# Kernel tuning notes

Measured on AMD Instinct MI355X. Metric: run time of the kernel, lower is better.

Reference implementation:

```python
import jax, jax.numpy as jnp
import numpy as np

N = 50000        # nodes
E = 1_600_000    # edges (avg degree 32)
F_IN = 128       # node feature dim
H = 64           # hidden_channels
C = 19           # output classes
G = 512          # graphs in the batch


def setup_inputs() -> dict:
    key = jax.random.key(0)
    ks = jax.random.split(key, 9)
    x = jax.random.normal(ks[0], (N, F_IN), dtype=jnp.float32)
    edge_index = jax.random.randint(ks[1], (2, E), 0, N, dtype=jnp.int64)
    batch = jnp.sort(jax.random.randint(ks[2], (N,), 0, G, dtype=jnp.int64))
    W1 = jax.random.normal(ks[3], (F_IN, H), dtype=jnp.float32) / np.sqrt(F_IN)
    b1 = jnp.zeros((H,), dtype=jnp.float32)
    W2 = jax.random.normal(ks[4], (H, H), dtype=jnp.float32) / np.sqrt(H)
    b2 = jnp.zeros((H,), dtype=jnp.float32)
    W_out = jax.random.normal(ks[5], (H, C), dtype=jnp.float32) / np.sqrt(H)
    b_out = jnp.zeros((C,), dtype=jnp.float32)
    return {"x": x, "edge_index": edge_index, "batch": batch,
            "W1": W1, "b1": b1, "W2": W2, "b2": b2,
            "W_out": W_out, "b_out": b_out}


def _gcn_conv(x, src, dst, W, b, n_nodes):
    """PyG GCNConv: add self-loops, symmetric D^-1/2 (A+I) D^-1/2 norm,
    linear transform first, gather-scale-scatter aggregation, then bias."""
    x = x @ W  # [N, out]
    loop = jnp.arange(n_nodes, dtype=src.dtype)
    s = jnp.concatenate([src, loop])  # source (message origin)
    d = jnp.concatenate([dst, loop])  # target (aggregation site)
    deg = jax.ops.segment_sum(jnp.ones_like(d, dtype=x.dtype), d,
                              num_segments=n_nodes)
    dinv = jnp.where(deg > 0, jax.lax.rsqrt(deg), 0.0)
    norm = dinv[s] * dinv[d]                       # [E+N]
    msg = x[s] * norm[:, None]                     # gather + scale
    out = jax.ops.segment_sum(msg, d, num_segments=n_nodes)  # scatter-add
    return out + b


def reference(x, edge_index, batch, W1, b1, W2, b2, W_out, b_out):
    src, dst = edge_index[0], edge_index[1]
    h = _gcn_conv(x, src, dst, W1, b1, N)
    h = jax.nn.relu(h)
    # F.dropout(training=False) -> identity (eval mode)
    h = _gcn_conv(h, src, dst, W2, b2, N)
    # global mean pool over graphs
    sums = jax.ops.segment_sum(h, batch, num_segments=G)        # [G, H]
    cnts = jax.ops.segment_sum(jnp.ones((N,), h.dtype), batch,
                               num_segments=G)                  # [G]
    pooled = sums / jnp.maximum(cnts, 1.0)[:, None]
    return pooled @ W_out + b_out                               # [G, C]
```

## Files before the change

kernel.cpp:

```cpp
#include <hip/hip_runtime.h>
#include <hip/hip_bf16.h>

#define F_IN 128
#define HID  64
#define NCLS 19
#define BW   128
#define NBMAX 512
#define ACAP 3072
#define BCAP 8192
#define BKCAP 5120
#define W1STR 136
#define W2STR 72

typedef __bf16 bf16x8 __attribute__((ext_vector_type(8)));
typedef float  f32x4  __attribute__((ext_vector_type(4)));

__device__ __forceinline__ float ldf(const void* p, long i, int fp32) {
    if (fp32) return ((const float*)p)[i];
    return __bfloat162float(((const __hip_bfloat16*)p)[i]);
}
__device__ __forceinline__ int ldi(const void* p, long i, int i64) {
    if (i64) return (int)((const long long*)p)[i];
    return ((const int*)p)[i];
}
__device__ __forceinline__ unsigned short f2bf(float f) {
    __hip_bfloat16 h = __float2bfloat16(f);
    unsigned short r;
    __builtin_memcpy(&r, &h, 2);
    return r;
}
__device__ __forceinline__ float bflo(unsigned u) { return __uint_as_float(u << 16); }
__device__ __forceinline__ float bfhi(unsigned u) { return __uint_as_float(u & 0xffff0000u); }

__device__ __forceinline__ bf16x8 ldfrag(const unsigned short* p) {
    uint4 u = *(const uint4*)p;
    return __builtin_bit_cast(bf16x8, u);
}
__device__ __forceinline__ bf16x8 ldfrag_any(const void* p, long off, int fp32) {
    if (!fp32) return ldfrag((const unsigned short*)p + off);
    const float* f = (const float*)p + off;
    unsigned short s[8];
#pragma unroll
    for (int i = 0; i < 8; ++i) s[i] = f2bf(f[i]);
    uint4 u = make_uint4((unsigned)s[0] | ((unsigned)s[1] << 16),
                         (unsigned)s[2] | ((unsigned)s[3] << 16),
                         (unsigned)s[4] | ((unsigned)s[5] << 16),
                         (unsigned)s[6] | ((unsigned)s[7] << 16));
    return __builtin_bit_cast(bf16x8, u);
}

__global__ __launch_bounds__(512) void k_detect(const void* x, const void* ei, int* flags,
                                                int* __restrict__ bcur, int NB) {
    int t = threadIdx.x;
    for (int b = t; b < NB; b += 512) bcur[b] = b * BKCAP;
    if (t != 0) return;
    const unsigned* xw = (const unsigned*)x;
    int bf16 = 1;
    for (int i = 0; i < 16; ++i) {
        unsigned w = xw[i];
        int elo = (w >> 7) & 0xFF;
        int ehi = (w >> 23) & 0xFF;
        if (elo < 100 || elo > 140 || ehi < 100 || ehi > 140) bf16 = 0;
    }
    const unsigned* iw = (const unsigned*)ei;
    int i64 = 1; unsigned anyev = 0;
    for (int k = 0; k < 8; ++k) {
        if (iw[2 * k + 1] != 0) i64 = 0;
        anyev |= iw[2 * k];
    }
    if (anyev == 0) i64 = 0;
    flags[0] = bf16 ? 0 : 1;
    flags[1] = i64;
}

__global__ __launch_bounds__(256) void k_bounds(const void* __restrict__ batch, int N, int G,
                                                int* __restrict__ bounds,
                                                const int* __restrict__ flags) {
    int i64 = flags[1];
    int i = blockIdx.x * 256 + threadIdx.x;
    if (i >= N) return;
    int b = min(max(ldi(batch, i, i64), 0), G - 1);
    int p = (i == 0) ? -1 : min(max(ldi(batch, (long)i - 1, i64), 0), G - 1);
    for (int g = p + 1; g <= b; ++g) bounds[g] = i;
    if (i == N - 1)
        for (int g = b + 1; g <= G; ++g) bounds[g] = N;
}

__global__ __launch_bounds__(512) void k_sortA(const void* __restrict__ ei, int E, int nbuck,
                                               int* bcur, int* __restrict__ bkt,
                                               const int* __restrict__ flags) {
    __shared__ int lbuf[ACAP];
    __shared__ unsigned short lbkt[ACAP];
    __shared__ int lh[NBMAX];
    __shared__ int lsc[NBMAX];
    __shared__ int lcur[NBMAX];
    __shared__ int gbase[NBMAX];
    int i64 = flags[1];
    int t = threadIdx.x;
    int e0 = blockIdx.x * ACAP;
    int e1 = min(E, e0 + ACAP);
    int cnt = e1 - e0;
    lh[t] = 0;
    __syncthreads();
    for (int e = e0 + t; e < e1; e += 512)
        atomicAdd(&lh[(ldi(ei, (long)E + e, i64) >> 7) & (NBMAX - 1)], 1);
    __syncthreads();
    int v = lh[t];
    lsc[t] = v;
    __syncthreads();
    for (int off = 1; off < 512; off <<= 1) {
        int a = (t >= off) ? lsc[t - off] : 0;
        __syncthreads();
        lsc[t] += a;
        __syncthreads();
    }
    int ex = lsc[t] - v;
    lsc[t] = ex;
    lcur[t] = ex;
    gbase[t] = (v && t < nbuck) ? atomicAdd(&bcur[t], v) : 0;
    __syncthreads();
    for (int e = e0 + t; e < e1; e += 512) {
        int s = ldi(ei, e, i64);
        int d = ldi(ei, (long)E + e, i64);
        int b = (d >> 7) & (NBMAX - 1);
        int r = atomicAdd(&lcur[b], 1);
        r = min(max(r, 0), ACAP - 1);
        lbuf[r] = (s << 7) | (d & (BW - 1));
        lbkt[r] = (unsigned short)b;
    }
    __syncthreads();
    for (int i = t; i < cnt; i += 512) {
        int lo = lbkt[i];
        int idx = gbase[lo] + (i - lsc[lo]);
        if (idx >= lo * BKCAP && idx < (lo + 1) * BKCAP) bkt[idx] = lbuf[i];
    }
}

__global__ __launch_bounds__(256) void k_sortB(const int* __restrict__ bkt,
                                               const int* __restrict__ bcur,
                                               int N,
                                               int* __restrict__ csr,
                                               int* __restrict__ cursor,
                                               int* __restrict__ deg,
                                               float* __restrict__ dinv) {
    __shared__ int lcsr[BCAP];
    __shared__ int lh[BW], lsc[BW], lcur[BW];
    int b = blockIdx.x, t = threadIdx.x;
    int base = b * BKCAP;
    int cnt = min(max(bcur[b] - base, 0), BKCAP);
    int end = base + cnt;
    if (t < BW) lh[t] = 0;
    __syncthreads();
    for (int i = base + t; i < end; i += 256)
        atomicAdd(&lh[bkt[i] & (BW - 1)], 1);
    __syncthreads();
    if (t < BW) lsc[t] = lh[t];
    __syncthreads();
    for (int off = 1; off < BW; off <<= 1) {
        int a = (t < BW && t >= off) ? lsc[t - off] : 0;
        __syncthreads();
        if (t < BW) lsc[t] += a;
        __syncthreads();
    }
    if (t < BW) {
        int ex = lsc[t] - lh[t];
        lcur[t] = ex;
        int n = b * BW + t;
        if (n < N) {
            cursor[n] = base + ex;
            deg[n] = lh[t];
            dinv[n] = rsqrtf((float)(lh[t] + 1));
        }
    }
    __syncthreads();
    bool fits = (cnt <= BCAP);
    for (int i = base + t; i < end; i += 256) {
        int w = bkt[i];
        int r = atomicAdd(&lcur[w & (BW - 1)], 1);
        int sv = (int)((unsigned)w >> 7);
        if (sv >= N) sv = 0;
        if (fits) { r = min(max(r, 0), BCAP - 1); lcsr[r] = sv; }
        else { r = min(max(r, 0), BKCAP - 1); csr[base + r] = sv; }
    }
    __syncthreads();
    if (fits)
        for (int i = t; i < cnt; i += 256) csr[base + i] = lcsr[i];
}

__global__ __launch_bounds__(256) void k_gemm1(const void* __restrict__ x,
                                               const void* __restrict__ W,
                                               const float* __restrict__ dinv,
                                               unsigned short* __restrict__ t, int N,
                                               const int* __restrict__ flags) {
    __shared__ __align__(16) unsigned short wt[HID * W1STR];
    int fp32 = flags[0];
    int tid = threadIdx.x;
    for (int i = tid; i < F_IN * HID; i += 256) {
        int k = i >> 6, n = i & 63;
        wt[n * W1STR + k] = f2bf(ldf(W, i, fp32));
    }
    __syncthreads();
    int wv = tid >> 6, lane = tid & 63;
    int quad = lane >> 4, l16 = lane & 15;
    int r0 = blockIdx.x * 64 + wv * 16;
    int rowA = min(r0 + l16, N - 1);
    bf16x8 a[4];
#pragma unroll
    for (int kq = 0; kq < 4; ++kq)
        a[kq] = ldfrag_any(x, (long)rowA * F_IN + kq * 32 + quad * 8, fp32);
    float di[4];
    int rowC = r0 + quad * 4;
#pragma unroll
    for (int r = 0; r < 4; ++r) di[r] = (rowC + r < N) ? dinv[rowC + r] : 0.f;
#pragma unroll
    for (int cg = 0; cg < 4; ++cg) {
        int col = cg * 16 + l16;
        f32x4 acc = {0.f, 0.f, 0.f, 0.f};
#pragma unroll
        for (int kq = 0; kq < 4; ++kq) {
            bf16x8 b = ldfrag(wt + col * W1STR + kq * 32 + quad * 8);
            acc = __builtin_amdgcn_mfma_f32_16x16x32_bf16(a[kq], b, acc, 0, 0, 0);
        }
#pragma unroll
        for (int r = 0; r < 4; ++r) {
            int row = rowC + r;
            if (row < N) t[(size_t)row * HID + col] = f2bf(di[r] * acc[r]);
        }
    }
}

__global__ __launch_bounds__(256) void k_gemm2(const unsigned short* __restrict__ h,
                                               const void* __restrict__ W,
                                               const float* __restrict__ dinv,
                                               unsigned short* __restrict__ t, int N,
                                               const int* __restrict__ flags) {
    __shared__ __align__(16) unsigned short wt[HID * W2STR];
    int fp32 = flags[0];
    int tid = threadIdx.x;
    for (int i = tid; i < HID * HID; i += 256) {
        int k = i >> 6, n = i & 63;
        wt[n * W2STR + k] = f2bf(ldf(W, i, fp32));
    }
    __syncthreads();
    int wv = tid >> 6, lane = tid & 63;
    int quad = lane >> 4, l16 = lane & 15;
    int r0 = blockIdx.x * 64 + wv * 16;
    int rowA = min(r0 + l16, N - 1);
    bf16x8 a[2];
#pragma unroll
    for (int kq = 0; kq < 2; ++kq)
        a[kq] = ldfrag(h + (size_t)rowA * HID + kq * 32 + quad * 8);
    float di[4];
    int rowC = r0 + quad * 4;
#pragma unroll
    for (int r = 0; r < 4; ++r) di[r] = (rowC + r < N) ? dinv[rowC + r] : 0.f;
#pragma unroll
    for (int cg = 0; cg < 4; ++cg) {
        int col = cg * 16 + l16;
        f32x4 acc = {0.f, 0.f, 0.f, 0.f};
#pragma unroll
        for (int kq = 0; kq < 2; ++kq) {
            bf16x8 b = ldfrag(wt + col * W2STR + kq * 32 + quad * 8);
            acc = __builtin_amdgcn_mfma_f32_16x16x32_bf16(a[kq], b, acc, 0, 0, 0);
        }
#pragma unroll
        for (int r = 0; r < 4; ++r) {
            int row = rowC + r;
            if (row < N) t[(size_t)row * HID + col] = f2bf(di[r] * acc[r]);
        }
    }
}

template <bool RELU>
__global__ __launch_bounds__(256) void k_agg(const unsigned short* __restrict__ t,
                                             const int* __restrict__ csr,
                                             const int* __restrict__ cursor,
                                             const int* __restrict__ deg,
                                             const float* __restrict__ dinv,
                                             const void* __restrict__ bias,
                                             unsigned short* __restrict__ out,
                                             int N, int SZ, const int* __restrict__ flags) {
    int node = blockIdx.x * 4 + (threadIdx.x >> 6);
    if (node >= N) return;
    int lane = threadIdx.x & 63;
    int g = lane >> 3;
    int l8 = (lane & 7) * 8;
    int beg = cursor[node];
    int dg = deg[node];
    beg = min(max(beg, 0), SZ);
    int end = beg + min(max(dg, 0), SZ - beg);
    float a0 = 0.f, a1 = 0.f, a2 = 0.f, a3 = 0.f;
    float a4 = 0.f, a5 = 0.f, a6 = 0.f, a7 = 0.f;
    for (int e = beg; e < end; e += 32) {
        int i0 = e + g, i1 = e + 8 + g, i2 = e + 16 + g, i3 = e + 24 + g;
        int s0 = csr[i0 < end ? i0 : end - 1];
        int s1 = csr[i1 < end ? i1 : end - 1];
        int s2 = csr[i2 < end ? i2 : end - 1];
        int s3 = csr[i3 < end ? i3 : end - 1];
        s0 = ((unsigned)s0 < (unsigned)N) ? s0 : 0;
        s1 = ((unsigned)s1 < (unsigned)N) ? s1 : 0;
        s2 = ((unsigned)s2 < (unsigned)N) ? s2 : 0;
        s3 = ((unsigned)s3 < (unsigned)N) ? s3 : 0;
        uint4 v0 = *(const uint4*)(t + s0 * HID + l8);
        uint4 v1 = *(const uint4*)(t + s1 * HID + l8);
        uint4 v2 = *(const uint4*)(t + s2 * HID + l8);
        uint4 v3 = *(const uint4*)(t + s3 * HID + l8);
        if (i0 < end) {
            a0 += bflo(v0.x); a1 += bfhi(v0.x); a2 += bflo(v0.y); a3 += bfhi(v0.y);
            a4 += bflo(v0.z); a5 += bfhi(v0.z); a6 += bflo(v0.w); a7 += bfhi(v0.w);
        }
        if (i1 < end) {
            a0 += bflo(v1.x); a1 += bfhi(v1.x); a2 += bflo(v1.y); a3 += bfhi(v1.y);
            a4 += bflo(v1.z); a5 += bfhi(v1.z); a6 += bflo(v1.w); a7 += bfhi(v1.w);
        }
        if (i2 < end) {
            a0 += bflo(v2.x); a1 += bfhi(v2.x); a2 += bflo(v2.y); a3 += bfhi(v2.y);
            a4 += bflo(v2.z); a5 += bfhi(v2.z); a6 += bflo(v2.w); a7 += bfhi(v2.w);
        }
        if (i3 < end) {
            a0 += bflo(v3.x); a1 += bfhi(v3.x); a2 += bflo(v3.y); a3 += bfhi(v3.y);
            a4 += bflo(v3.z); a5 += bfhi(v3.z); a6 += bflo(v3.w); a7 += bfhi(v3.w);
        }
    }
#pragma unroll
    for (int m = 8; m <= 32; m <<= 1) {
        a0 += __shfl_xor(a0, m); a1 += __shfl_xor(a1, m);
        a2 += __shfl_xor(a2, m); a3 += __shfl_xor(a3, m);
        a4 += __shfl_xor(a4, m); a5 += __shfl_xor(a5, m);
        a6 += __shfl_xor(a6, m); a7 += __shfl_xor(a7, m);
    }
    uint4 sv = *(const uint4*)(t + node * HID + l8);
    a0 += bflo(sv.x); a1 += bfhi(sv.x); a2 += bflo(sv.y); a3 += bfhi(sv.y);
    a4 += bflo(sv.z); a5 += bfhi(sv.z); a6 += bflo(sv.w); a7 += bfhi(sv.w);
    int fp32 = flags[0];
    float di = dinv[node];
    float v0 = di * a0 + ldf(bias, l8 + 0, fp32);
    float v1 = di * a1 + ldf(bias, l8 + 1, fp32);
    float v2 = di * a2 + ldf(bias, l8 + 2, fp32);
    float v3 = di * a3 + ldf(bias, l8 + 3, fp32);
    float v4 = di * a4 + ldf(bias, l8 + 4, fp32);
    float v5 = di * a5 + ldf(bias, l8 + 5, fp32);
    float v6 = di * a6 + ldf(bias, l8 + 6, fp32);
    float v7 = di * a7 + ldf(bias, l8 + 7, fp32);
    if (RELU) {
        v0 = fmaxf(v0, 0.f); v1 = fmaxf(v1, 0.f); v2 = fmaxf(v2, 0.f); v3 = fmaxf(v3, 0.f);
        v4 = fmaxf(v4, 0.f); v5 = fmaxf(v5, 0.f); v6 = fmaxf(v6, 0.f); v7 = fmaxf(v7, 0.f);
    }
    if (g == 0) {
        uint4 pk;
        pk.x = (unsigned)f2bf(v0) | ((unsigned)f2bf(v1) << 16);
        pk.y = (unsigned)f2bf(v2) | ((unsigned)f2bf(v3) << 16);
        pk.z = (unsigned)f2bf(v4) | ((unsigned)f2bf(v5) << 16);
        pk.w = (unsigned)f2bf(v6) | ((unsigned)f2bf(v7) << 16);
        *(uint4*)(out + node * HID + l8) = pk;
    }
}

__global__ __launch_bounds__(64) void k_poolout(const unsigned short* __restrict__ h2,
                                                const int* __restrict__ bounds, int N,
                                                const void* __restrict__ Wout,
                                                const void* __restrict__ bout,
                                                void* __restrict__ out,
                                                const int* __restrict__ flags) {
    __shared__ float pr[HID];
    int g = blockIdx.x;
    int start = min(max(bounds[g], 0), N);
    int endg = min(max(bounds[g + 1], start), N);
    int lane = threadIdx.x;
    int half = lane >> 5;
    int l = lane & 31;
    float s0 = 0.f, s1 = 0.f;
    for (int r = start; r < endg; r += 4) {
        int r0 = r + half;
        int r1 = r + 2 + half;
        unsigned u0 = (r0 < endg) ? *(const unsigned*)(h2 + (size_t)r0 * HID + 2 * l) : 0u;
        unsigned u1 = (r1 < endg) ? *(const unsigned*)(h2 + (size_t)r1 * HID + 2 * l) : 0u;
        s0 += bflo(u0) + bflo(u1);
        s1 += bfhi(u0) + bfhi(u1);
    }
    s0 += __shfl_xor(s0, 32);
    s1 += __shfl_xor(s1, 32);
    if (lane < 32) {
        float inv = 1.f / fmaxf((float)(endg - start), 1.f);
        pr[2 * l] = s0 * inv;
        pr[2 * l + 1] = s1 * inv;
    }
    __syncthreads();
    int fp32 = flags[0];
    if (lane < NCLS) {
        float acc = ldf(bout, lane, fp32);
#pragma unroll 4
        for (int k = 0; k < HID; ++k)
            acc += pr[k] * ldf(Wout, k * NCLS + lane, fp32);
        if (fp32) ((float*)out)[g * NCLS + lane] = acc;
        else ((__hip_bfloat16*)out)[g * NCLS + lane] = __float2bfloat16(acc);
    }
}

extern "C" void kernel_launch(void* const* d_in, const int* in_sizes, int n_in,
                              void* d_out, int out_size, void* d_ws, size_t ws_size,
                              hipStream_t stream) {
    const void* x    = d_in[0];
    const void* ei   = d_in[1];
    const void* bat  = d_in[2];
    const void* W1   = d_in[3];
    const void* b1   = d_in[4];
    const void* W2   = d_in[5];
    const void* b2   = d_in[6];
    const void* Wout = d_in[7];
    const void* bout = d_in[8];

    const int N = in_sizes[0] / F_IN;
    const int E = in_sizes[1] / 2;
    const int G = out_size / NCLS;
    const int NB = (N + BW - 1) / BW;
    const int SZ = NB * BKCAP;

    char* ws = (char*)d_ws;
    size_t off = 0;
    auto carve = [&](size_t bytes) -> void* {
        void* p = ws + off;
        off = (off + bytes + 255) & ~(size_t)255;
        return p;
    };
    int*            flags  = (int*)carve(64);
    int*            deg    = (int*)carve((size_t)N * 4);
    int*            cursor = (int*)carve((size_t)N * 4);
    float*          dinv   = (float*)carve((size_t)N * 4);
    int*            bcur   = (int*)carve((size_t)NB * 4);
    int*            bounds = (int*)carve((size_t)(G + 1) * 4);
    int*            csr    = (int*)carve((size_t)SZ * 4);
    int*            bkt    = (int*)carve((size_t)SZ * 4);
    unsigned short* t      = (unsigned short*)carve((size_t)N * HID * 2);
    unsigned short* h      = (unsigned short*)carve((size_t)N * HID * 2);
    (void)ws_size; (void)n_in;

    k_detect<<<1, 512, 0, stream>>>(x, ei, flags, bcur, NB);
    k_bounds<<<(N + 255) / 256, 256, 0, stream>>>(bat, N, G, bounds, flags);

    int na = (E + ACAP - 1) / ACAP;
    k_sortA<<<na, 512, 0, stream>>>(ei, E, NB, bcur, bkt, flags);
    k_sortB<<<NB, 256, 0, stream>>>(bkt, bcur, N, csr, cursor, deg, dinv);

    int gb = (N + 63) / 64;
    int ab = (N + 3) / 4;
    k_gemm1<<<gb, 256, 0, stream>>>(x, W1, dinv, t, N, flags);
    k_agg<true><<<ab, 256, 0, stream>>>(t, csr, cursor, deg, dinv, b1, h, N, SZ, flags);
    k_gemm2<<<gb, 256, 0, stream>>>(h, W2, dinv, t, N, flags);
    k_agg<false><<<ab, 256, 0, stream>>>(t, csr, cursor, deg, dinv, b2, h, N, SZ, flags);
    k_poolout<<<G, 64, 0, stream>>>(h, bounds, N, Wout, bout, d_out, flags);
}
```

Before: 246.0 us.

## Use half-wave per node in aggregation, vectorize weight loads, widen pooling

The aggregation kernel now assigns a 32-lane half-wave to each node (8 nodes per block). It stages cursor, degree, dinv and bias in shared memory, prefetches the self-loop row early, and issues 8 independent gathers per iteration instead of 4. Weight staging and fp32 input fragments use float4 loads. The pooling kernel goes from 64 to 256 threads with a shared-memory reduction. Together these aim to raise memory-level parallelism and cut redundant global loads, but fewer lanes per node means longer per-node loops for high-degree nodes.

```diff
diff --git a/kernel.cpp b/kernel.cpp
--- a/kernel.cpp
+++ b/kernel.cpp
@@ -38,14 +38,13 @@
 }
 __device__ __forceinline__ bf16x8 ldfrag_any(const void* p, long off, int fp32) {
     if (!fp32) return ldfrag((const unsigned short*)p + off);
-    const float* f = (const float*)p + off;
-    unsigned short s[8];
-#pragma unroll
-    for (int i = 0; i < 8; ++i) s[i] = f2bf(f[i]);
-    uint4 u = make_uint4((unsigned)s[0] | ((unsigned)s[1] << 16),
-                         (unsigned)s[2] | ((unsigned)s[3] << 16),
-                         (unsigned)s[4] | ((unsigned)s[5] << 16),
-                         (unsigned)s[6] | ((unsigned)s[7] << 16));
+    const float4* f = (const float4*)((const float*)p + off);
+    float4 u0 = f[0];
+    float4 u1 = f[1];
+    uint4 u = make_uint4((unsigned)f2bf(u0.x) | ((unsigned)f2bf(u0.y) << 16),
+                         (unsigned)f2bf(u0.z) | ((unsigned)f2bf(u0.w) << 16),
+                         (unsigned)f2bf(u1.x) | ((unsigned)f2bf(u1.y) << 16),
+                         (unsigned)f2bf(u1.z) | ((unsigned)f2bf(u1.w) << 16));
     return __builtin_bit_cast(bf16x8, u);
 }
 
@@ -195,9 +194,21 @@
     __shared__ __align__(16) unsigned short wt[HID * W1STR];
     int fp32 = flags[0];
     int tid = threadIdx.x;
-    for (int i = tid; i < F_IN * HID; i += 256) {
-        int k = i >> 6, n = i & 63;
-        wt[n * W1STR + k] = f2bf(ldf(W, i, fp32));
+    if (fp32) {
+        const float* wf = (const float*)W;
+        for (int i = tid * 4; i < F_IN * HID; i += 1024) {
+            float4 w4 = *(const float4*)(wf + i);
+            int k = i >> 6, n = i & 63;
+            wt[(n + 0) * W1STR + k] = f2bf(w4.x);
+            wt[(n + 1) * W1STR + k] = f2bf(w4.y);
+            wt[(n + 2) * W1STR + k] = f2bf(w4.z);
+            wt[(n + 3) * W1STR + k] = f2bf(w4.w);
+        }
+    } else {
+        for (int i = tid; i < F_IN * HID; i += 256) {
+            int k = i >> 6, n = i & 63;
+            wt[n * W1STR + k] = f2bf(ldf(W, i, 0));
+        }
     }
     __syncthreads();
     int wv = tid >> 6, lane = tid & 63;
@@ -237,9 +248,21 @@
     __shared__ __align__(16) unsigned short wt[HID * W2STR];
     int fp32 = flags[0];
     int tid = threadIdx.x;
-    for (int i = tid; i < HID * HID; i += 256) {
-        int k = i >> 6, n = i & 63;
-        wt[n * W2STR + k] = f2bf(ldf(W, i, fp32));
+    if (fp32) {
+        const float* wf = (const float*)W;
+        for (int i = tid * 4; i < HID * HID; i += 1024) {
+            float4 w4 = *(const float4*)(wf + i);
+            int k = i >> 6, n = i & 63;
+            wt[(n + 0) * W2STR + k] = f2bf(w4.x);
+            wt[(n + 1) * W2STR + k] = f2bf(w4.y);
+            wt[(n + 2) * W2STR + k] = f2bf(w4.z);
+            wt[(n + 3) * W2STR + k] = f2bf(w4.w);
+        }
+    } else {
+        for (int i = tid; i < HID * HID; i += 256) {
+            int k = i >> 6, n = i & 63;
+            wt[n * W2STR + k] = f2bf(ldf(W, i, 0));
+        }
     }
     __syncthreads();
     int wv = tid >> 6, lane = tid & 63;
@@ -280,120 +303,134 @@
                                              const void* __restrict__ bias,
                                              unsigned short* __restrict__ out,
                                              int N, int SZ, const int* __restrict__ flags) {
-    int node = blockIdx.x * 4 + (threadIdx.x >> 6);
-    if (node >= N) return;
-    int lane = threadIdx.x & 63;
-    int g = lane >> 3;
-    int l8 = (lane & 7) * 8;
-    int beg = cursor[node];
-    int dg = deg[node];
+    __shared__ float sbias[HID];
+    __shared__ int scur[8];
+    __shared__ int sdeg[8];
+    __shared__ float sdv[8];
+    int tid = threadIdx.x;
+    int nb = blockIdx.x * 8;
+    if (tid < HID) sbias[tid] = ldf(bias, tid, flags[0]);
+    if (tid >= 64 && tid < 72) {
+        int q = tid - 64;
+        int node = nb + q;
+        int c = 0, d = 0;
+        float dv = 0.f;
+        if (node < N) { c = cursor[node]; d = deg[node]; dv = dinv[node]; }
+        scur[q] = c; sdeg[q] = d; sdv[q] = dv;
+    }
+    __syncthreads();
+    int wv = tid >> 6, lane = tid & 63;
+    int half = lane >> 5;
+    int idx = wv * 2 + half;
+    int node = nb + idx;
+    int l = lane & 31;
+    int g = l >> 3;
+    int l8 = (l & 7) * 8;
+    bool alive = (node < N);
+    int snode = alive ? node : 0;
+    int beg = scur[idx];
+    int dg = sdeg[idx];
     beg = min(max(beg, 0), SZ);
     int end = beg + min(max(dg, 0), SZ - beg);
+    uint4 sv = make_uint4(0u, 0u, 0u, 0u);
+    if (g == 0) sv = *(const uint4*)(t + (size_t)snode * HID + l8);
     float a0 = 0.f, a1 = 0.f, a2 = 0.f, a3 = 0.f;
     float a4 = 0.f, a5 = 0.f, a6 = 0.f, a7 = 0.f;
     for (int e = beg; e < end; e += 32) {
-        int i0 = e + g, i1 = e + 8 + g, i2 = e + 16 + g, i3 = e + 24 + g;
-        int s0 = csr[i0 < end ? i0 : end - 1];
-        int s1 = csr[i1 < end ? i1 : end - 1];
-        int s2 = csr[i2 < end ? i2 : end - 1];
-        int s3 = csr[i3 < end ? i3 : end - 1];
-        s0 = ((unsigned)s0 < (unsigned)N) ? s0 : 0;
-        s1 = ((unsigned)s1 < (unsigned)N) ? s1 : 0;
-        s2 = ((unsigned)s2 < (unsigned)N) ? s2 : 0;
-        s3 = ((unsigned)s3 < (unsigned)N) ? s3 : 0;
-        uint4 v0 = *(const uint4*)(t + s0 * HID + l8);
-        uint4 v1 = *(const uint4*)(t + s1 * HID + l8);
-        uint4 v2 = *(const uint4*)(t + s2 * HID + l8);
-        uint4 v3 = *(const uint4*)(t + s3 * HID + l8);
-        if (i0 < end) {
-            a0 += bflo(v0.x); a1 += bfhi(v0.x); a2 += bflo(v0.y); a3 += bfhi(v0.y);
-            a4 += bflo(v0.z); a5 += bfhi(v0.z); a6 += bflo(v0.w); a7 += bfhi(v0.w);
-        }
-        if (i1 < end) {
-            a0 += bflo(v1.x); a1 += bfhi(v1.x); a2 += bflo(v1.y); a3 += bfhi(v1.y);
-            a4 += bflo(v1.z); a5 += bfhi(v1.z); a6 += bflo(v1.w); a7 += bfhi(v1.w);
-        }
-        if (i2 < end) {
-            a0 += bflo(v2.x); a1 += bfhi(v2.x); a2 += bflo(v2.y); a3 += bfhi(v2.y);
-            a4 += bflo(v2.z); a5 += bfhi(v2.z); a6 += bflo(v2.w); a7 += bfhi(v2.w);
-        }
-        if (i3 < end) {
-            a0 += bflo(v3.x); a1 += bfhi(v3.x); a2 += bflo(v3.y); a3 += bfhi(v3.y);
-            a4 += bflo(v3.z); a5 += bfhi(v3.z); a6 += bflo(v3.w); a7 += bfhi(v3.w);
-        }
-    }
-#pragma unroll
-    for (int m = 8; m <= 32; m <<= 1) {
+        int s[8];
+#pragma unroll
+        for (int k = 0; k < 8; ++k) {
+            int i = e + 4 * k + g;
+            int si = csr[i < end ? i : end - 1];
+            s[k] = ((unsigned)si < (unsigned)N) ? si : 0;
+        }
+        uint4 v[8];
+#pragma unroll
+        for (int k = 0; k < 8; ++k)
+            v[k] = *(const uint4*)(t + (size_t)s[k] * HID + l8);
+#pragma unroll
+        for (int k = 0; k < 8; ++k) {
+            if (e + 4 * k + g < end) {
+                a0 += bflo(v[k].x); a1 += bfhi(v[k].x);
+                a2 += bflo(v[k].y); a3 += bfhi(v[k].y);
+                a4 += bflo(v[k].z); a5 += bfhi(v[k].z);
+                a6 += bflo(v[k].w); a7 += bfhi(v[k].w);
+            }
+        }
+    }
+#pragma unroll
+    for (int m = 8; m <= 16; m <<= 1) {
         a0 += __shfl_xor(a0, m); a1 += __shfl_xor(a1, m);
         a2 += __shfl_xor(a2, m); a3 += __shfl_xor(a3, m);
         a4 += __shfl_xor(a4, m); a5 += __shfl_xor(a5, m);
         a6 += __shfl_xor(a6, m); a7 += __shfl_xor(a7, m);
     }
-    uint4 sv = *(const uint4*)(t + node * HID + l8);
-    a0 += bflo(sv.x); a1 += bfhi(sv.x); a2 += bflo(sv.y); a3 += bfhi(sv.y);
-    a4 += bflo(sv.z); a5 += bfhi(sv.z); a6 += bflo(sv.w); a7 += bfhi(sv.w);
-    int fp32 = flags[0];
-    float di = dinv[node];
-    float v0 = di * a0 + ldf(bias, l8 + 0, fp32);
-    float v1 = di * a1 + ldf(bias, l8 + 1, fp32);
-    float v2 = di * a2 + ldf(bias, l8 + 2, fp32);
-    float v3 = di * a3 + ldf(bias, l8 + 3, fp32);
-    float v4 = di * a4 + ldf(bias, l8 + 4, fp32);
-    float v5 = di * a5 + ldf(bias, l8 + 5, fp32);
-    float v6 = di * a6 + ldf(bias, l8 + 6, fp32);
-    float v7 = di * a7 + ldf(bias, l8 + 7, fp32);
-    if (RELU) {
-        v0 = fmaxf(v0, 0.f); v1 = fmaxf(v1, 0.f); v2 = fmaxf(v2, 0.f); v3 = fmaxf(v3, 0.f);
-        v4 = fmaxf(v4, 0.f); v5 = fmaxf(v5, 0.f); v6 = fmaxf(v6, 0.f); v7 = fmaxf(v7, 0.f);
-    }
-    if (g == 0) {
+    if (g == 0 && alive) {
+        a0 += bflo(sv.x); a1 += bfhi(sv.x); a2 += bflo(sv.y); a3 += bfhi(sv.y);
+        a4 += bflo(sv.z); a5 += bfhi(sv.z); a6 += bflo(sv.w); a7 += bfhi(sv.w);
+        float di = sdv[idx];
+        float v0 = di * a0 + sbias[l8 + 0];
+        float v1 = di * a1 + sbias[l8 + 1];
+        float v2 = di * a2 + sbias[l8 + 2];
+        float v3 = di * a3 + sbias[l8 + 3];
+        float v4 = di * a4 + sbias[l8 + 4];
+        float v5 = di * a5 + sbias[l8 + 5];
+        float v6 = di * a6 + sbias[l8 + 6];
+        float v7 = di * a7 + sbias[l8 + 7];
+        if (RELU) {
+            v0 = fmaxf(v0, 0.f); v1 = fmaxf(v1, 0.f); v2 = fmaxf(v2, 0.f); v3 = fmaxf(v3, 0.f);
+            v4 = fmaxf(v4, 0.f); v5 = fmaxf(v5, 0.f); v6 = fmaxf(v6, 0.f); v7 = fmaxf(v7, 0.f);
+        }
         uint4 pk;
         pk.x = (unsigned)f2bf(v0) | ((unsigned)f2bf(v1) << 16);
         pk.y = (unsigned)f2bf(v2) | ((unsigned)f2bf(v3) << 16);
         pk.z = (unsigned)f2bf(v4) | ((unsigned)f2bf(v5) << 16);
         pk.w = (unsigned)f2bf(v6) | ((unsigned)f2bf(v7) << 16);
-        *(uint4*)(out + node * HID + l8) = pk;
-    }
-}
-
-__global__ __launch_bounds__(64) void k_poolout(const unsigned short* __restrict__ h2,
-                                                const int* __restrict__ bounds, int N,
-                                                const void* __restrict__ Wout,
-                                                const void* __restrict__ bout,
-                                                void* __restrict__ out,
-                                                const int* __restrict__ flags) {
+        *(uint4*)(out + (size_t)node * HID + l8) = pk;
+    }
+}
+
+__global__ __launch_bounds__(256) void k_poolout(const unsigned short* __restrict__ h2,
+                                                 const int* __restrict__ bounds, int N,
+                                                 const void* __restrict__ Wout,
+                                                 const void* __restrict__ bout,
+                                                 void* __restrict__ out,
+                                                 const int* __restrict__ flags) {
     __shared__ float pr[HID];
+    __shared__ float sacc[4][HID];
     int g = blockIdx.x;
     int start = min(max(bounds[g], 0), N);
     int endg = min(max(bounds[g + 1], start), N);
-    int lane = threadIdx.x;
+    int tid = threadIdx.x;
+    int wv = tid >> 6, lane = tid & 63;
     int half = lane >> 5;
     int l = lane & 31;
     float s0 = 0.f, s1 = 0.f;
-    for (int r = start; r < endg; r += 4) {
-        int r0 = r + half;
-        int r1 = r + 2 + half;
-        unsigned u0 = (r0 < endg) ? *(const unsigned*)(h2 + (size_t)r0 * HID + 2 * l) : 0u;
-        unsigned u1 = (r1 < endg) ? *(const unsigned*)(h2 + (size_t)r1 * HID + 2 * l) : 0u;
-        s0 += bflo(u0) + bflo(u1);
-        s1 += bfhi(u0) + bfhi(u1);
+    for (int r = start + wv * 2 + half; r < endg; r += 8) {
+        unsigned u = *(const unsigned*)(h2 + (size_t)r * HID + 2 * l);
+        s0 += bflo(u);
+        s1 += bfhi(u);
     }
     s0 += __shfl_xor(s0, 32);
     s1 += __shfl_xor(s1, 32);
     if (lane < 32) {
+        sacc[wv][2 * l] = s0;
+        sacc[wv][2 * l + 1] = s1;
+    }
+    __syncthreads();
+    if (tid < HID) {
         float inv = 1.f / fmaxf((float)(endg - start), 1.f);
-        pr[2 * l] = s0 * inv;
-        pr[2 * l + 1] = s1 * inv;
+        pr[tid] = (sacc[0][tid] + sacc[1][tid] + sacc[2][tid] + sacc[3][tid]) * inv;
     }
     __syncthreads();
     int fp32 = flags[0];
-    if (lane < NCLS) {
-        float acc = ldf(bout, lane, fp32);
+    if (tid < NCLS) {
+        float acc = ldf(bout, tid, fp32);
 #pragma unroll 4
         for (int k = 0; k < HID; ++k)
-            acc += pr[k] * ldf(Wout, k * NCLS + lane, fp32);
-        if (fp32) ((float*)out)[g * NCLS + lane] = acc;
-        else ((__hip_bfloat16*)out)[g * NCLS + lane] = __float2bfloat16(acc);
+            acc += pr[k] * ldf(Wout, k * NCLS + tid, fp32);
+        if (fp32) ((float*)out)[g * NCLS + tid] = acc;
+        else ((__hip_bfloat16*)out)[g * NCLS + tid] = __float2bfloat16(acc);
     }
 }
 
@@ -443,10 +480,10 @@
     k_sortB<<<NB, 256, 0, stream>>>(bkt, bcur, N, csr, cursor, deg, dinv);
 
     int gb = (N + 63) / 64;
-    int ab = (N + 3) / 4;
+    int ab = (N + 7) / 8;
     k_gemm1<<<gb, 256, 0, stream>>>(x, W1, dinv, t, N, flags);
     k_agg<true><<<ab, 256, 0, stream>>>(t, csr, cursor, deg, dinv, b1, h, N, SZ, flags);
     k_gemm2<<<gb, 256, 0, stream>>>(h, W2, dinv, t, N, flags);
     k_agg<false><<<ab, 256, 0, stream>>>(t, csr, cursor, deg, dinv, b2, h, N, SZ, flags);
-    k_poolout<<<G, 64, 0, stream>>>(h, bounds, N, Wout, bout, d_out, flags);
-}
+    k_poolout<<<G, 256, 0, stream>>>(h, bounds, N, Wout, bout, d_out, flags);
+}
```

New measurement: 205.7 us. 16.4% less time.
